# Kernel optimization log

Measured on AMD Instinct MI355X. Metric: run time of the kernel, lower is better.

Reference implementation:

```python
import jax, jax.numpy as jnp
import numpy as np

N_NODES = 50000
N_EDGES = 800000
IN_FEATS, N_HIDDEN, N_CLASSES = 128, 128, 64
N_LAYERS = 3  # total GraphConv layers = N_LAYERS + 1


def setup_inputs() -> dict:
    key = jax.random.key(0)
    ks = jax.random.split(key, 16)
    features = jax.random.normal(ks[0], (N_NODES, IN_FEATS), dtype=jnp.float32)
    src = jax.random.randint(ks[1], (N_EDGES,), 0, N_NODES, dtype=jnp.int32)
    dst = jax.random.randint(ks[2], (N_EDGES,), 0, N_NODES, dtype=jnp.int32)
    def lin(k, fan_in, fan_out):
        s = 1.0 / np.sqrt(fan_in)
        return jax.random.uniform(k, (fan_in, fan_out), jnp.float32, -s, s)
    dims = [IN_FEATS] + [N_HIDDEN] * N_LAYERS + [N_CLASSES]
    inp = {"features": features, "src": src, "dst": dst}
    for i in range(len(dims) - 1):
        inp[f"W{i}"] = lin(ks[3 + i], dims[i], dims[i + 1])
        inp[f"b{i}"] = jnp.zeros((dims[i + 1],), jnp.float32)
    inp["Wp"] = lin(ks[10], N_CLASSES, 1)
    inp["bp"] = jnp.zeros((1,), jnp.float32)
    inp["Wv"] = lin(ks[11], N_CLASSES, 1)
    inp["bv"] = jnp.zeros((1,), jnp.float32)
    return inp


def _graph_conv(h, src, dst, norm_src, norm_dst, W, b, activate):
    # DGL GraphConv, norm='both': D_out^{-1/2} A D_in^{-1/2} X W + b
    h = h * norm_src  # [N, d]
    msg = h[src]      # [E, d] gather
    agg = jax.ops.segment_sum(msg, dst, num_segments=N_NODES)  # [N, d] scatter-add
    out = agg * norm_dst @ W + b
    return jax.nn.relu(out) if activate else out


def reference(features, src, dst, W0, b0, W1, b1, W2, b2, W3, b3, Wp, bp, Wv, bv):
    ones = jnp.ones((N_EDGES,), jnp.float32)
    out_deg = jax.ops.segment_sum(ones, src, num_segments=N_NODES)
    in_deg = jax.ops.segment_sum(ones, dst, num_segments=N_NODES)
    norm_src = jnp.clip(out_deg, 1.0) ** -0.5  # [N]
    norm_dst = jnp.clip(in_deg, 1.0) ** -0.5
    norm_src = norm_src[:, None]
    norm_dst = norm_dst[:, None]
    Ws = [W0, W1, W2, W3]
    bs = [b0, b1, b2, b3]
    h = features
    for i in range(4):
        h = _graph_conv(h, src, dst, norm_src, norm_dst, Ws[i], bs[i], activate=(i < 3))
    mN = jnp.sum(h, axis=0, keepdims=True)  # readout_nodes sum -> [1, n_classes]
    PI = h @ Wp + bp   # [N, 1]
    V = mN @ Wv + bv   # [1, 1]
    return (PI, V)
```

## Files before the change

kernel.cpp:

```cpp
#include <hip/hip_runtime.h>
#include <cstddef>

#define N_NODES 50000
#define N_EDGES 800000
#define NBUK    196
#define NBLK    256
#define EPB     3125
#define HEAD_BLOCKS 3136

typedef unsigned u32;
typedef unsigned short u16;
typedef __attribute__((ext_vector_type(8))) short bf16x8;
typedef __attribute__((ext_vector_type(4))) float f32x4;

__device__ __forceinline__ float bflo(u32 u) { return __uint_as_float(u << 16); }
__device__ __forceinline__ float bfhi(u32 u) { return __uint_as_float(u & 0xFFFF0000u); }
__device__ __forceinline__ u32 f2bf(float f) {
    u32 u = __float_as_uint(f);
    return (u + 0x7FFFu + ((u >> 16) & 1u)) >> 16;
}
__device__ __forceinline__ u32 packbf2(float a, float b) { return f2bf(a) | (f2bf(b) << 16); }

#define OFF_NS    0u
#define OFF_ND    200000u
#define OFF_RS    400000u
#define OFF_ES    600016u
#define OFF_CNTD  3800016u
#define OFF_CNTS  4000720u
#define OFF_TOTD  4201424u
#define OFF_TOTS  4202208u
#define OFF_BASED 4202992u
#define OFF_BASES 4203776u
#define OFF_VP    4204560u
#define OFF_DB    4217104u
#define OFF_SB    10617104u
#define OFF_T0    13817104u
#define OFF_T1    26617104u
#define OFF_TA    39417104u
#define OFF_TT    52217104u

__global__ __launch_bounds__(256)
void p1_kernel(const int* __restrict__ src, const int* __restrict__ dst,
               u32* __restrict__ cntD, u32* __restrict__ cntS) {
    __shared__ u32 dc[NBUK], sc[NBUK];
    int b = blockIdx.x, tid = threadIdx.x;
    if (tid < NBUK) { dc[tid] = 0; sc[tid] = 0; }
    __syncthreads();
    int lo = b * EPB, hi = lo + EPB;
    for (int e = lo + tid; e < hi; e += 256) {
        atomicAdd(&dc[dst[e] >> 8], 1u);
        atomicAdd(&sc[src[e] >> 8], 1u);
    }
    __syncthreads();
    if (tid < NBUK) {
        cntD[b * NBUK + tid] = dc[tid];
        cntS[b * NBUK + tid] = sc[tid];
    }
}

__global__ __launch_bounds__(256)
void p2a_kernel(u32* __restrict__ cntD, u32* __restrict__ cntS,
                u32* __restrict__ totD, u32* __restrict__ totS) {
    __shared__ u32 sc[256];
    int k = blockIdx.x, tid = threadIdx.x;
    u32 v = cntD[tid * NBUK + k];
    sc[tid] = v;
    __syncthreads();
    for (int o = 1; o < 256; o <<= 1) {
        u32 t = (tid >= o) ? sc[tid - o] : 0u;
        __syncthreads(); sc[tid] += t; __syncthreads();
    }
    cntD[tid * NBUK + k] = sc[tid] - v;
    if (tid == 255) totD[k] = sc[255];
    __syncthreads();
    v = cntS[tid * NBUK + k];
    sc[tid] = v;
    __syncthreads();
    for (int o = 1; o < 256; o <<= 1) {
        u32 t = (tid >= o) ? sc[tid - o] : 0u;
        __syncthreads(); sc[tid] += t; __syncthreads();
    }
    cntS[tid * NBUK + k] = sc[tid] - v;
    if (tid == 255) totS[k] = sc[255];
}

__global__ __launch_bounds__(256)
void p2b_kernel(const u32* __restrict__ totD, const u32* __restrict__ totS,
                u32* __restrict__ baseD, u32* __restrict__ baseS, u32* __restrict__ rs) {
    __shared__ u32 sc[256];
    int tid = threadIdx.x;
    u32 v = (tid < NBUK) ? totD[tid] : 0u;
    sc[tid] = v;
    __syncthreads();
    for (int o = 1; o < 256; o <<= 1) {
        u32 t = (tid >= o) ? sc[tid - o] : 0u;
        __syncthreads(); sc[tid] += t; __syncthreads();
    }
    if (tid < NBUK) baseD[tid] = sc[tid] - v;
    __syncthreads();
    v = (tid < NBUK) ? totS[tid] : 0u;
    sc[tid] = v;
    __syncthreads();
    for (int o = 1; o < 256; o <<= 1) {
        u32 t = (tid >= o) ? sc[tid - o] : 0u;
        __syncthreads(); sc[tid] += t; __syncthreads();
    }
    if (tid < NBUK) baseS[tid] = sc[tid] - v;
    if (tid == 0) rs[N_NODES] = N_EDGES;
}

__global__ __launch_bounds__(256)
void p3_kernel(const int* __restrict__ src, const int* __restrict__ dst,
               const u32* __restrict__ cntD, const u32* __restrict__ cntS,
               const u32* __restrict__ baseD, const u32* __restrict__ baseS,
               int2* __restrict__ db, int* __restrict__ sb) {
    __shared__ u32 od[NBUK], os[NBUK];
    int b = blockIdx.x, tid = threadIdx.x;
    if (tid < NBUK) {
        od[tid] = baseD[tid] + cntD[b * NBUK + tid];
        os[tid] = baseS[tid] + cntS[b * NBUK + tid];
    }
    __syncthreads();
    int lo = b * EPB, hi = lo + EPB;
    for (int e = lo + tid; e < hi; e += 256) {
        int s = src[e], d = dst[e];
        u32 p = atomicAdd(&od[d >> 8], 1u);
        db[p] = make_int2(s, d);
        u32 q = atomicAdd(&os[s >> 8], 1u);
        sb[q] = s;
    }
}

__global__ __launch_bounds__(256)
void p4d_kernel(const int2* __restrict__ db, const u32* __restrict__ totD,
                const u32* __restrict__ baseD, float* __restrict__ nd,
                u32* __restrict__ rs, int* __restrict__ es) {
    __shared__ u32 hist[256], sc[256], off[256];
    int k = blockIdx.x, tid = threadIdx.x;
    hist[tid] = 0;
    __syncthreads();
    u32 nEd = totD[k], base = baseD[k];
    for (u32 i = tid; i < nEd; i += 256)
        atomicAdd(&hist[db[base + i].y & 255], 1u);
    __syncthreads();
    u32 v = hist[tid];
    sc[tid] = v;
    __syncthreads();
    for (int o = 1; o < 256; o <<= 1) {
        u32 t = (tid >= o) ? sc[tid - o] : 0u;
        __syncthreads(); sc[tid] += t; __syncthreads();
    }
    u32 pf = sc[tid] - v;
    int node = k * 256 + tid;
    if (node < N_NODES) {
        rs[node] = base + pf;
        u32 c = v < 1u ? 1u : v;
        nd[node] = rsqrtf((float)c);
    }
    off[tid] = base + pf;
    __syncthreads();
    for (u32 i = tid; i < nEd; i += 256) {
        int2 p = db[base + i];
        u32 pos = atomicAdd(&off[p.y & 255], 1u);
        es[pos] = p.x;
    }
}

__global__ __launch_bounds__(256)
void p4s_kernel(const int* __restrict__ sb, const u32* __restrict__ totS,
                const u32* __restrict__ baseS, float* __restrict__ ns) {
    __shared__ u32 hist[256];
    int k = blockIdx.x, tid = threadIdx.x;
    hist[tid] = 0;
    __syncthreads();
    u32 n = totS[k], base = baseS[k];
    for (u32 i = tid; i < n; i += 256)
        atomicAdd(&hist[sb[base + i] & 255], 1u);
    __syncthreads();
    int node = k * 256 + tid;
    if (node < N_NODES) {
        u32 c = hist[tid]; if (c < 1u) c = 1u;
        ns[node] = rsqrtf((float)c);
    }
}

__global__ __launch_bounds__(256)
void prescale_kernel(const float* __restrict__ feat, const float* __restrict__ ns,
                     u16* __restrict__ hS) {
    int i = blockIdx.x * 256 + threadIdx.x;
    if (i < N_NODES * 32) {
        float s = ns[i >> 5];
        float4 v = *(const float4*)&feat[(size_t)i * 4];
        uint2 o;
        o.x = packbf2(s * v.x, s * v.y);
        o.y = packbf2(s * v.z, s * v.w);
        *(uint2*)&hS[(size_t)i * 4] = o;
    }
}

__global__ __launch_bounds__(256)
void agg128_kernel(const u16* __restrict__ h, const u32* __restrict__ rs,
                   const int* __restrict__ es, u16* __restrict__ agg) {
    int node = blockIdx.x * 4 + (threadIdx.x >> 6);
    int lane = threadIdx.x & 63;
    int quarter = lane >> 4;
    int q = lane & 15;
    const uint4* hp = (const uint4*)h;
    u32 s0 = rs[node], s1 = rs[node + 1];
    float acc[8] = {0.f, 0.f, 0.f, 0.f, 0.f, 0.f, 0.f, 0.f};
    u32 i = s0;
    for (; i + 16 <= s1; i += 16) {
        int e0 = es[i + quarter],     e1 = es[i + 4 + quarter];
        int e2 = es[i + 8 + quarter], e3 = es[i + 12 + quarter];
        uint4 a = hp[(size_t)e0 * 16 + q];
        uint4 b = hp[(size_t)e1 * 16 + q];
        uint4 c = hp[(size_t)e2 * 16 + q];
        uint4 d = hp[(size_t)e3 * 16 + q];
        acc[0] += (bflo(a.x) + bflo(b.x)) + (bflo(c.x) + bflo(d.x));
        acc[1] += (bfhi(a.x) + bfhi(b.x)) + (bfhi(c.x) + bfhi(d.x));
        acc[2] += (bflo(a.y) + bflo(b.y)) + (bflo(c.y) + bflo(d.y));
        acc[3] += (bfhi(a.y) + bfhi(b.y)) + (bfhi(c.y) + bfhi(d.y));
        acc[4] += (bflo(a.z) + bflo(b.z)) + (bflo(c.z) + bflo(d.z));
        acc[5] += (bfhi(a.z) + bfhi(b.z)) + (bfhi(c.z) + bfhi(d.z));
        acc[6] += (bflo(a.w) + bflo(b.w)) + (bflo(c.w) + bflo(d.w));
        acc[7] += (bfhi(a.w) + bfhi(b.w)) + (bfhi(c.w) + bfhi(d.w));
    }
    for (; i + 4 <= s1; i += 4) {
        uint4 a = hp[(size_t)es[i + quarter] * 16 + q];
        acc[0] += bflo(a.x); acc[1] += bfhi(a.x);
        acc[2] += bflo(a.y); acc[3] += bfhi(a.y);
        acc[4] += bflo(a.z); acc[5] += bfhi(a.z);
        acc[6] += bflo(a.w); acc[7] += bfhi(a.w);
    }
    u32 rem = s1 - i;
    if ((u32)quarter < rem) {
        uint4 a = hp[(size_t)es[i + quarter] * 16 + q];
        acc[0] += bflo(a.x); acc[1] += bfhi(a.x);
        acc[2] += bflo(a.y); acc[3] += bfhi(a.y);
        acc[4] += bflo(a.z); acc[5] += bfhi(a.z);
        acc[6] += bflo(a.w); acc[7] += bfhi(a.w);
    }
    #pragma unroll
    for (int j = 0; j < 8; ++j) {
        acc[j] += __shfl_xor(acc[j], 16, 64);
        acc[j] += __shfl_xor(acc[j], 32, 64);
    }
    if (lane < 16) {
        uint4 pk;
        pk.x = packbf2(acc[0], acc[1]);
        pk.y = packbf2(acc[2], acc[3]);
        pk.z = packbf2(acc[4], acc[5]);
        pk.w = packbf2(acc[6], acc[7]);
        *(uint4*)&agg[(size_t)node * 128 + q * 8] = pk;
    }
}

template <int NCOL, int MODE>
__global__ __launch_bounds__(256)
void mfma_gemm_kernel(const u16* __restrict__ Ab, const float* __restrict__ W,
                      const float* __restrict__ bias, const float* __restrict__ ns,
                      const float* __restrict__ nd, u16* __restrict__ C) {
    constexpr int NT = NCOL / 16;
    constexpr int WROW = 136;
    constexpr int CROW = NCOL + 4;
    __shared__ u16 Wt[NCOL * WROW];
    __shared__ float Cl[4][16 * CROW];
    int tid = threadIdx.x;
    int w = tid >> 6, lane = tid & 63;
    int rowbase = blockIdx.x * 64 + w * 16;

    for (int i = tid; i < 128 * NCOL; i += 256) {
        int k = i / NCOL, c = i % NCOL;
        Wt[c * WROW + k] = (u16)f2bf(W[i]);
    }
    __syncthreads();

    int m = lane & 15, kb = lane >> 4;
    int arow = rowbase + m;
    if (arow > N_NODES - 1) arow = N_NODES - 1;
    f32x4 acc[NT];
    #pragma unroll
    for (int nt = 0; nt < NT; ++nt) acc[nt] = (f32x4){0.f, 0.f, 0.f, 0.f};

    #pragma unroll
    for (int ks = 0; ks < 4; ++ks) {
        int k0 = ks * 32 + kb * 8;
        bf16x8 a = *(const bf16x8*)&Ab[(size_t)arow * 128 + k0];
        #pragma unroll
        for (int nt = 0; nt < NT; ++nt) {
            bf16x8 b = *(const bf16x8*)&Wt[(nt * 16 + m) * WROW + k0];
            acc[nt] = __builtin_amdgcn_mfma_f32_16x16x32_bf16(a, b, acc[nt], 0, 0, 0);
        }
    }

    #pragma unroll
    for (int nt = 0; nt < NT; ++nt)
        #pragma unroll
        for (int reg = 0; reg < 4; ++reg)
            Cl[w][(kb * 4 + reg) * CROW + nt * 16 + m] = acc[nt][reg];
    __syncthreads();

    constexpr int CQ = NCOL / 4;
    for (int i = lane; i < 16 * CQ; i += 64) {
        int r = i / CQ, c4 = (i % CQ) * 4;
        int row = rowbase + r;
        if (row < N_NODES) {
            float4 o = *(float4*)&Cl[w][r * CROW + c4];
            if (MODE == 0) {
                float sd = nd[row], ss = ns[row];
                o.x = ss * fmaxf(sd * o.x + bias[c4 + 0], 0.f);
                o.y = ss * fmaxf(sd * o.y + bias[c4 + 1], 0.f);
                o.z = ss * fmaxf(sd * o.z + bias[c4 + 2], 0.f);
                o.w = ss * fmaxf(sd * o.w + bias[c4 + 3], 0.f);
            }
            uint2 pk = {packbf2(o.x, o.y), packbf2(o.z, o.w)};
            *(uint2*)&C[(size_t)row * NCOL + c4] = pk;
        }
    }
}

__global__ __launch_bounds__(256)
void l3head_kernel(const u16* __restrict__ t, const u32* __restrict__ rs,
                   const int* __restrict__ es, const float* __restrict__ nd,
                   const float* __restrict__ b3, const float* __restrict__ Wp,
                   const float* __restrict__ Wv, const float* __restrict__ bp,
                   float* __restrict__ out, float* __restrict__ vpart) {
    __shared__ float sv;
    if (threadIdx.x == 0) sv = 0.f;
    __syncthreads();
    int lane = threadIdx.x & 63;
    int wvid = threadIdx.x >> 6;
    int quarter = lane >> 4;
    int q = lane & 15;
    const uint2* hp = (const uint2*)t;
    float4 b3v = ((const float4*)b3)[q];
    float4 wpv = ((const float4*)Wp)[q];
    float4 wvv = ((const float4*)Wv)[q];
    float bpv = bp[0];
    float vacc = 0.f;
    for (int n = blockIdx.x * 4 + wvid; n < N_NODES; n += HEAD_BLOCKS * 4) {
        u32 s0 = rs[n], s1 = rs[n + 1];
        float4 acc = {0.f, 0.f, 0.f, 0.f};
        u32 i = s0;
        for (; i + 8 <= s1; i += 8) {
            int e0 = es[i + quarter], e1 = es[i + 4 + quarter];
            uint2 a = hp[(size_t)e0 * 16 + q];
            uint2 b = hp[(size_t)e1 * 16 + q];
            acc.x += bflo(a.x) + bflo(b.x);
            acc.y += bfhi(a.x) + bfhi(b.x);
            acc.z += bflo(a.y) + bflo(b.y);
            acc.w += bfhi(a.y) + bfhi(b.y);
        }
        for (; i + 4 <= s1; i += 4) {
            int e = es[i + quarter];
            uint2 a = hp[(size_t)e * 16 + q];
            acc.x += bflo(a.x); acc.y += bfhi(a.x);
            acc.z += bflo(a.y); acc.w += bfhi(a.y);
        }
        u32 rem = s1 - i;
        if ((u32)quarter < rem) {
            int e = es[i + quarter];
            uint2 a = hp[(size_t)e * 16 + q];
            acc.x += bflo(a.x); acc.y += bfhi(a.x);
            acc.z += bflo(a.y); acc.w += bfhi(a.y);
        }
        acc.x += __shfl_xor(acc.x, 16, 64); acc.x += __shfl_xor(acc.x, 32, 64);
        acc.y += __shfl_xor(acc.y, 16, 64); acc.y += __shfl_xor(acc.y, 32, 64);
        acc.z += __shfl_xor(acc.z, 16, 64); acc.z += __shfl_xor(acc.z, 32, 64);
        acc.w += __shfl_xor(acc.w, 16, 64); acc.w += __shfl_xor(acc.w, 32, 64);
        float ndv = nd[n];
        float4 h;
        h.x = ndv * acc.x + b3v.x;
        h.y = ndv * acc.y + b3v.y;
        h.z = ndv * acc.z + b3v.z;
        h.w = ndv * acc.w + b3v.w;
        float p  = h.x * wpv.x + h.y * wpv.y + h.z * wpv.z + h.w * wpv.w;
        float vv = h.x * wvv.x + h.y * wvv.y + h.z * wvv.z + h.w * wvv.w;
        p  += __shfl_xor(p, 1, 64);  p  += __shfl_xor(p, 2, 64);
        p  += __shfl_xor(p, 4, 64);  p  += __shfl_xor(p, 8, 64);
        vv += __shfl_xor(vv, 1, 64); vv += __shfl_xor(vv, 2, 64);
        vv += __shfl_xor(vv, 4, 64); vv += __shfl_xor(vv, 8, 64);
        if (lane == 0) { out[n] = p + bpv; vacc += vv; }
    }
    if (lane == 0) atomicAdd(&sv, vacc);
    __syncthreads();
    if (threadIdx.x == 0) vpart[blockIdx.x] = sv;
}

__global__ __launch_bounds__(256)
void vred_kernel(const float* __restrict__ vpart, const float* __restrict__ bv,
                 float* __restrict__ out) {
    float v = 0.f;
    for (int i = threadIdx.x; i < HEAD_BLOCKS; i += 256) v += vpart[i];
    #pragma unroll
    for (int off = 32; off; off >>= 1) v += __shfl_down(v, off, 64);
    __shared__ float s[4];
    if ((threadIdx.x & 63) == 0) s[threadIdx.x >> 6] = v;
    __syncthreads();
    if (threadIdx.x == 0) out[N_NODES] = s[0] + s[1] + s[2] + s[3] + bv[0];
}

extern "C" void kernel_launch(void* const* d_in, const int* in_sizes, int n_in,
                              void* d_out, int out_size, void* d_ws, size_t ws_size,
                              hipStream_t stream) {
    const float* feat = (const float*)d_in[0];
    const int*   src  = (const int*)d_in[1];
    const int*   dst  = (const int*)d_in[2];
    const float* W0 = (const float*)d_in[3];  const float* b0 = (const float*)d_in[4];
    const float* W1 = (const float*)d_in[5];  const float* b1 = (const float*)d_in[6];
    const float* W2 = (const float*)d_in[7];  const float* b2 = (const float*)d_in[8];
    const float* W3 = (const float*)d_in[9];  const float* b3 = (const float*)d_in[10];
    const float* Wp = (const float*)d_in[11]; const float* bp = (const float*)d_in[12];
    const float* Wv = (const float*)d_in[13]; const float* bv = (const float*)d_in[14];
    float* out = (float*)d_out;
    char*  wsb = (char*)d_ws;

    float* ns    = (float*)(wsb + OFF_NS);
    float* nd    = (float*)(wsb + OFF_ND);
    u32*   rs    = (u32*)(wsb + OFF_RS);
    int*   es    = (int*)(wsb + OFF_ES);
    u32*   cntD  = (u32*)(wsb + OFF_CNTD);
    u32*   cntS  = (u32*)(wsb + OFF_CNTS);
    u32*   totD  = (u32*)(wsb + OFF_TOTD);
    u32*   totS  = (u32*)(wsb + OFF_TOTS);
    u32*   baseD = (u32*)(wsb + OFF_BASED);
    u32*   baseS = (u32*)(wsb + OFF_BASES);
    float* vpart = (float*)(wsb + OFF_VP);
    int2*  db    = (int2*)(wsb + OFF_DB);
    int*   sb    = (int*)(wsb + OFF_SB);
    u16*   T0    = (u16*)(wsb + OFF_T0);
    u16*   T1    = (u16*)(wsb + OFF_T1);
    u16*   TA    = (u16*)(wsb + OFF_TA);
    u16*   Tt    = (u16*)(wsb + OFF_TT);

    p1_kernel<<<NBLK, 256, 0, stream>>>(src, dst, cntD, cntS);
    p2a_kernel<<<NBUK, 256, 0, stream>>>(cntD, cntS, totD, totS);
    p2b_kernel<<<1, 256, 0, stream>>>(totD, totS, baseD, baseS, rs);
    p3_kernel<<<NBLK, 256, 0, stream>>>(src, dst, cntD, cntS, baseD, baseS, db, sb);
    p4d_kernel<<<NBUK, 256, 0, stream>>>(db, totD, baseD, nd, rs, es);
    p4s_kernel<<<NBUK, 256, 0, stream>>>(sb, totS, baseS, ns);

    prescale_kernel<<<6250, 256, 0, stream>>>(feat, ns, T0);

    agg128_kernel<<<12500, 256, 0, stream>>>(T0, rs, es, TA);
    mfma_gemm_kernel<128, 0><<<782, 256, 0, stream>>>(TA, W0, b0, ns, nd, T1);
    agg128_kernel<<<12500, 256, 0, stream>>>(T1, rs, es, TA);
    mfma_gemm_kernel<128, 0><<<782, 256, 0, stream>>>(TA, W1, b1, ns, nd, T0);
    agg128_kernel<<<12500, 256, 0, stream>>>(T0, rs, es, TA);
    mfma_gemm_kernel<128, 0><<<782, 256, 0, stream>>>(TA, W2, b2, ns, nd, T1);
    mfma_gemm_kernel<64, 1><<<782, 256, 0, stream>>>(T1, W3, b3, ns, nd, Tt);
    l3head_kernel<<<HEAD_BLOCKS, 256, 0, stream>>>(Tt, rs, es, nd, b3, Wp, Wv, bp, out, vpart);
    vred_kernel<<<1, 256, 0, stream>>>(vpart, bv, out);
}
```

Before: 343.3 us.

## Fuse prescale into degree kernel, mask-based gather loops, wider head gathers

Folds the feature prescale into the source-degree kernel so each bucket block computes its norms into shared memory and writes the scaled bf16 features, saving a launch and the ns read-back. The aggregation and head kernels swap their multi-stage tail loops for a single 16/32-edge loop that clamps out-of-range indices and multiplies those contributions by zero. The head now gathers 16-byte chunks with 8 edges in flight per step. The GEMM weight staging packs two bf16 values per 32-bit shared store. The cost is that the fused prescale runs on only 196 blocks, and low-degree nodes now issue wasted masked loads.

```diff
diff --git a/kernel.cpp b/kernel.cpp
--- a/kernel.cpp
+++ b/kernel.cpp
@@ -167,9 +167,11 @@
 }
 
 __global__ __launch_bounds__(256)
-void p4s_kernel(const int* __restrict__ sb, const u32* __restrict__ totS,
-                const u32* __restrict__ baseS, float* __restrict__ ns) {
+void p4sp_kernel(const int* __restrict__ sb, const u32* __restrict__ totS,
+                 const u32* __restrict__ baseS, float* __restrict__ ns,
+                 const float* __restrict__ feat, u16* __restrict__ hS) {
     __shared__ u32 hist[256];
+    __shared__ float sns[256];
     int k = blockIdx.x, tid = threadIdx.x;
     hist[tid] = 0;
     __syncthreads();
@@ -178,23 +180,23 @@
         atomicAdd(&hist[sb[base + i] & 255], 1u);
     __syncthreads();
     int node = k * 256 + tid;
-    if (node < N_NODES) {
+    {
         u32 c = hist[tid]; if (c < 1u) c = 1u;
-        ns[node] = rsqrtf((float)c);
-    }
-}
-
-__global__ __launch_bounds__(256)
-void prescale_kernel(const float* __restrict__ feat, const float* __restrict__ ns,
-                     u16* __restrict__ hS) {
-    int i = blockIdx.x * 256 + threadIdx.x;
-    if (i < N_NODES * 32) {
-        float s = ns[i >> 5];
-        float4 v = *(const float4*)&feat[(size_t)i * 4];
+        float s = rsqrtf((float)c);
+        sns[tid] = s;
+        if (node < N_NODES) ns[node] = s;
+    }
+    __syncthreads();
+    for (int i = tid; i < 256 * 32; i += 256) {
+        int r = i >> 5, c4 = i & 31;
+        int g = k * 256 + r;
+        if (g >= N_NODES) break;
+        float s = sns[r];
+        float4 v = *(const float4*)&feat[(size_t)g * 128 + c4 * 4];
         uint2 o;
         o.x = packbf2(s * v.x, s * v.y);
         o.y = packbf2(s * v.z, s * v.w);
-        *(uint2*)&hS[(size_t)i * 4] = o;
+        *(uint2*)&hS[(size_t)g * 128 + c4 * 4] = o;
     }
 }
 
@@ -203,42 +205,33 @@
                    const int* __restrict__ es, u16* __restrict__ agg) {
     int node = blockIdx.x * 4 + (threadIdx.x >> 6);
     int lane = threadIdx.x & 63;
-    int quarter = lane >> 4;
+    int grp = lane >> 4;
     int q = lane & 15;
     const uint4* hp = (const uint4*)h;
     u32 s0 = rs[node], s1 = rs[node + 1];
+    u32 deg = s1 - s0;
+    u32 last = deg ? deg - 1u : 0u;
     float acc[8] = {0.f, 0.f, 0.f, 0.f, 0.f, 0.f, 0.f, 0.f};
-    u32 i = s0;
-    for (; i + 16 <= s1; i += 16) {
-        int e0 = es[i + quarter],     e1 = es[i + 4 + quarter];
-        int e2 = es[i + 8 + quarter], e3 = es[i + 12 + quarter];
+    for (u32 b = 0; b < deg; b += 16) {
+        u32 p0 = b + grp, p1 = b + 4 + grp, p2 = b + 8 + grp, p3 = b + 12 + grp;
+        float m0 = p0 < deg ? 1.f : 0.f;  u32 x0 = p0 < deg ? p0 : last;
+        float m1 = p1 < deg ? 1.f : 0.f;  u32 x1 = p1 < deg ? p1 : last;
+        float m2 = p2 < deg ? 1.f : 0.f;  u32 x2 = p2 < deg ? p2 : last;
+        float m3 = p3 < deg ? 1.f : 0.f;  u32 x3 = p3 < deg ? p3 : last;
+        int e0 = es[s0 + x0], e1 = es[s0 + x1];
+        int e2 = es[s0 + x2], e3 = es[s0 + x3];
         uint4 a = hp[(size_t)e0 * 16 + q];
-        uint4 b = hp[(size_t)e1 * 16 + q];
+        uint4 bb = hp[(size_t)e1 * 16 + q];
         uint4 c = hp[(size_t)e2 * 16 + q];
         uint4 d = hp[(size_t)e3 * 16 + q];
-        acc[0] += (bflo(a.x) + bflo(b.x)) + (bflo(c.x) + bflo(d.x));
-        acc[1] += (bfhi(a.x) + bfhi(b.x)) + (bfhi(c.x) + bfhi(d.x));
-        acc[2] += (bflo(a.y) + bflo(b.y)) + (bflo(c.y) + bflo(d.y));
-        acc[3] += (bfhi(a.y) + bfhi(b.y)) + (bfhi(c.y) + bfhi(d.y));
-        acc[4] += (bflo(a.z) + bflo(b.z)) + (bflo(c.z) + bflo(d.z));
-        acc[5] += (bfhi(a.z) + bfhi(b.z)) + (bfhi(c.z) + bfhi(d.z));
-        acc[6] += (bflo(a.w) + bflo(b.w)) + (bflo(c.w) + bflo(d.w));
-        acc[7] += (bfhi(a.w) + bfhi(b.w)) + (bfhi(c.w) + bfhi(d.w));
-    }
-    for (; i + 4 <= s1; i += 4) {
-        uint4 a = hp[(size_t)es[i + quarter] * 16 + q];
-        acc[0] += bflo(a.x); acc[1] += bfhi(a.x);
-        acc[2] += bflo(a.y); acc[3] += bfhi(a.y);
-        acc[4] += bflo(a.z); acc[5] += bfhi(a.z);
-        acc[6] += bflo(a.w); acc[7] += bfhi(a.w);
-    }
-    u32 rem = s1 - i;
-    if ((u32)quarter < rem) {
-        uint4 a = hp[(size_t)es[i + quarter] * 16 + q];
-        acc[0] += bflo(a.x); acc[1] += bfhi(a.x);
-        acc[2] += bflo(a.y); acc[3] += bfhi(a.y);
-        acc[4] += bflo(a.z); acc[5] += bfhi(a.z);
-        acc[6] += bflo(a.w); acc[7] += bfhi(a.w);
+        acc[0] += m0 * bflo(a.x) + m1 * bflo(bb.x) + m2 * bflo(c.x) + m3 * bflo(d.x);
+        acc[1] += m0 * bfhi(a.x) + m1 * bfhi(bb.x) + m2 * bfhi(c.x) + m3 * bfhi(d.x);
+        acc[2] += m0 * bflo(a.y) + m1 * bflo(bb.y) + m2 * bflo(c.y) + m3 * bflo(d.y);
+        acc[3] += m0 * bfhi(a.y) + m1 * bfhi(bb.y) + m2 * bfhi(c.y) + m3 * bfhi(d.y);
+        acc[4] += m0 * bflo(a.z) + m1 * bflo(bb.z) + m2 * bflo(c.z) + m3 * bflo(d.z);
+        acc[5] += m0 * bfhi(a.z) + m1 * bfhi(bb.z) + m2 * bfhi(c.z) + m3 * bfhi(d.z);
+        acc[6] += m0 * bflo(a.w) + m1 * bflo(bb.w) + m2 * bflo(c.w) + m3 * bflo(d.w);
+        acc[7] += m0 * bfhi(a.w) + m1 * bfhi(bb.w) + m2 * bfhi(c.w) + m3 * bfhi(d.w);
     }
     #pragma unroll
     for (int j = 0; j < 8; ++j) {
@@ -269,9 +262,11 @@
     int w = tid >> 6, lane = tid & 63;
     int rowbase = blockIdx.x * 64 + w * 16;
 
-    for (int i = tid; i < 128 * NCOL; i += 256) {
-        int k = i / NCOL, c = i % NCOL;
-        Wt[c * WROW + k] = (u16)f2bf(W[i]);
+    for (int i = tid; i < 64 * NCOL; i += 256) {
+        int k2 = i / NCOL, c = i % NCOL;
+        float w0 = W[(size_t)(2 * k2) * NCOL + c];
+        float w1 = W[(size_t)(2 * k2 + 1) * NCOL + c];
+        *(u32*)&Wt[c * WROW + 2 * k2] = packbf2(w0, w1);
     }
     __syncthreads();
 
@@ -330,56 +325,60 @@
     __syncthreads();
     int lane = threadIdx.x & 63;
     int wvid = threadIdx.x >> 6;
-    int quarter = lane >> 4;
-    int q = lane & 15;
-    const uint2* hp = (const uint2*)t;
-    float4 b3v = ((const float4*)b3)[q];
-    float4 wpv = ((const float4*)Wp)[q];
-    float4 wvv = ((const float4*)Wv)[q];
+    int oct = lane >> 3;
+    int q = lane & 7;
+    const uint4* hp = (const uint4*)t;
+    float4 b3a = ((const float4*)b3)[q * 2];
+    float4 b3b = ((const float4*)b3)[q * 2 + 1];
+    float4 wpa = ((const float4*)Wp)[q * 2];
+    float4 wpb = ((const float4*)Wp)[q * 2 + 1];
+    float4 wva = ((const float4*)Wv)[q * 2];
+    float4 wvb = ((const float4*)Wv)[q * 2 + 1];
     float bpv = bp[0];
     float vacc = 0.f;
     for (int n = blockIdx.x * 4 + wvid; n < N_NODES; n += HEAD_BLOCKS * 4) {
         u32 s0 = rs[n], s1 = rs[n + 1];
-        float4 acc = {0.f, 0.f, 0.f, 0.f};
-        u32 i = s0;
-        for (; i + 8 <= s1; i += 8) {
-            int e0 = es[i + quarter], e1 = es[i + 4 + quarter];
-            uint2 a = hp[(size_t)e0 * 16 + q];
-            uint2 b = hp[(size_t)e1 * 16 + q];
-            acc.x += bflo(a.x) + bflo(b.x);
-            acc.y += bfhi(a.x) + bfhi(b.x);
-            acc.z += bflo(a.y) + bflo(b.y);
-            acc.w += bfhi(a.y) + bfhi(b.y);
+        u32 deg = s1 - s0;
+        u32 last = deg ? deg - 1u : 0u;
+        float acc[8] = {0.f, 0.f, 0.f, 0.f, 0.f, 0.f, 0.f, 0.f};
+        for (u32 b = 0; b < deg; b += 32) {
+            u32 p0 = b + oct, p1 = b + 8 + oct, p2 = b + 16 + oct, p3 = b + 24 + oct;
+            float m0 = p0 < deg ? 1.f : 0.f;  u32 x0 = p0 < deg ? p0 : last;
+            float m1 = p1 < deg ? 1.f : 0.f;  u32 x1 = p1 < deg ? p1 : last;
+            float m2 = p2 < deg ? 1.f : 0.f;  u32 x2 = p2 < deg ? p2 : last;
+            float m3 = p3 < deg ? 1.f : 0.f;  u32 x3 = p3 < deg ? p3 : last;
+            int e0 = es[s0 + x0], e1 = es[s0 + x1];
+            int e2 = es[s0 + x2], e3 = es[s0 + x3];
+            uint4 a = hp[(size_t)e0 * 8 + q];
+            uint4 bb = hp[(size_t)e1 * 8 + q];
+            uint4 c = hp[(size_t)e2 * 8 + q];
+            uint4 d = hp[(size_t)e3 * 8 + q];
+            acc[0] += m0 * bflo(a.x) + m1 * bflo(bb.x) + m2 * bflo(c.x) + m3 * bflo(d.x);
+            acc[1] += m0 * bfhi(a.x) + m1 * bfhi(bb.x) + m2 * bfhi(c.x) + m3 * bfhi(d.x);
+            acc[2] += m0 * bflo(a.y) + m1 * bflo(bb.y) + m2 * bflo(c.y) + m3 * bflo(d.y);
+            acc[3] += m0 * bfhi(a.y) + m1 * bfhi(bb.y) + m2 * bfhi(c.y) + m3 * bfhi(d.y);
+            acc[4] += m0 * bflo(a.z) + m1 * bflo(bb.z) + m2 * bflo(c.z) + m3 * bflo(d.z);
+            acc[5] += m0 * bfhi(a.z) + m1 * bfhi(bb.z) + m2 * bfhi(c.z) + m3 * bfhi(d.z);
+            acc[6] += m0 * bflo(a.w) + m1 * bflo(bb.w) + m2 * bflo(c.w) + m3 * bflo(d.w);
+            acc[7] += m0 * bfhi(a.w) + m1 * bfhi(bb.w) + m2 * bfhi(c.w) + m3 * bfhi(d.w);
         }
-        for (; i + 4 <= s1; i += 4) {
-            int e = es[i + quarter];
-            uint2 a = hp[(size_t)e * 16 + q];
-            acc.x += bflo(a.x); acc.y += bfhi(a.x);
-            acc.z += bflo(a.y); acc.w += bfhi(a.y);
+        #pragma unroll
+        for (int j = 0; j < 8; ++j) {
+            acc[j] += __shfl_xor(acc[j], 8, 64);
+            acc[j] += __shfl_xor(acc[j], 16, 64);
+            acc[j] += __shfl_xor(acc[j], 32, 64);
         }
-        u32 rem = s1 - i;
-        if ((u32)quarter < rem) {
-            int e = es[i + quarter];
-            uint2 a = hp[(size_t)e * 16 + q];
-            acc.x += bflo(a.x); acc.y += bfhi(a.x);
-            acc.z += bflo(a.y); acc.w += bfhi(a.y);
-        }
-        acc.x += __shfl_xor(acc.x, 16, 64); acc.x += __shfl_xor(acc.x, 32, 64);
-        acc.y += __shfl_xor(acc.y, 16, 64); acc.y += __shfl_xor(acc.y, 32, 64);
-        acc.z += __shfl_xor(acc.z, 16, 64); acc.z += __shfl_xor(acc.z, 32, 64);
-        acc.w += __shfl_xor(acc.w, 16, 64); acc.w += __shfl_xor(acc.w, 32, 64);
         float ndv = nd[n];
-        float4 h;
-        h.x = ndv * acc.x + b3v.x;
-        h.y = ndv * acc.y + b3v.y;
-        h.z = ndv * acc.z + b3v.z;
-        h.w = ndv * acc.w + b3v.w;
-        float p  = h.x * wpv.x + h.y * wpv.y + h.z * wpv.z + h.w * wpv.w;
-        float vv = h.x * wvv.x + h.y * wvv.y + h.z * wvv.z + h.w * wvv.w;
-        p  += __shfl_xor(p, 1, 64);  p  += __shfl_xor(p, 2, 64);
-        p  += __shfl_xor(p, 4, 64);  p  += __shfl_xor(p, 8, 64);
-        vv += __shfl_xor(vv, 1, 64); vv += __shfl_xor(vv, 2, 64);
-        vv += __shfl_xor(vv, 4, 64); vv += __shfl_xor(vv, 8, 64);
+        float h0 = ndv * acc[0] + b3a.x, h1 = ndv * acc[1] + b3a.y;
+        float h2 = ndv * acc[2] + b3a.z, h3 = ndv * acc[3] + b3a.w;
+        float h4 = ndv * acc[4] + b3b.x, h5 = ndv * acc[5] + b3b.y;
+        float h6 = ndv * acc[6] + b3b.z, h7 = ndv * acc[7] + b3b.w;
+        float p  = h0 * wpa.x + h1 * wpa.y + h2 * wpa.z + h3 * wpa.w
+                 + h4 * wpb.x + h5 * wpb.y + h6 * wpb.z + h7 * wpb.w;
+        float vv = h0 * wva.x + h1 * wva.y + h2 * wva.z + h3 * wva.w
+                 + h4 * wvb.x + h5 * wvb.y + h6 * wvb.z + h7 * wvb.w;
+        p  += __shfl_xor(p, 1, 64);  p  += __shfl_xor(p, 2, 64);  p  += __shfl_xor(p, 4, 64);
+        vv += __shfl_xor(vv, 1, 64); vv += __shfl_xor(vv, 2, 64); vv += __shfl_xor(vv, 4, 64);
         if (lane == 0) { out[n] = p + bpv; vacc += vv; }
     }
     if (lane == 0) atomicAdd(&sv, vacc);
@@ -438,9 +437,7 @@
     p2b_kernel<<<1, 256, 0, stream>>>(totD, totS, baseD, baseS, rs);
     p3_kernel<<<NBLK, 256, 0, stream>>>(src, dst, cntD, cntS, baseD, baseS, db, sb);
     p4d_kernel<<<NBUK, 256, 0, stream>>>(db, totD, baseD, nd, rs, es);
-    p4s_kernel<<<NBUK, 256, 0, stream>>>(sb, totS, baseS, ns);
-
-    prescale_kernel<<<6250, 256, 0, stream>>>(feat, ns, T0);
+    p4sp_kernel<<<NBUK, 256, 0, stream>>>(sb, totS, baseS, ns, feat, T0);
 
     agg128_kernel<<<12500, 256, 0, stream>>>(T0, rs, es, TA);
     mfma_gemm_kernel<128, 0><<<782, 256, 0, stream>>>(TA, W0, b0, ns, nd, T1);
```

Result: slower. 350.6 us (+2.1%).
